# Performance work log

Hardware: AMD Instinct MI355X
Metric: run time of the kernel (lower is better)

## Reference

```python
import jax, jax.numpy as jnp
import numpy as np
from jax import lax


def _lstm_dir(x, w_ih, w_hh, b_ih, b_hh, reverse):
    """One direction of a PyTorch-style LSTM.

    x: [B, T, D]; w_ih: [4H, D]; w_hh: [4H, H]; gate order i, f, g, o.
    Returns hidden states [B, T, H] aligned with input timesteps (reverse
    scan stacks outputs back at their original positions, matching the
    backward direction of torch bidirectional LSTM).
    """
    B = x.shape[0]
    H = w_hh.shape[1]
    # Precompute input contribution for all timesteps: [T, B, 4H]
    gx = jnp.einsum('btd,gd->tbg', x, w_ih) + b_ih + b_hh

    def step(carry, g_t):
        h, c = carry
        g = g_t + h @ w_hh.T
        i, f, gg, o = jnp.split(g, 4, axis=-1)
        i = jax.nn.sigmoid(i)
        f = jax.nn.sigmoid(f)
        gg = jnp.tanh(gg)
        o = jax.nn.sigmoid(o)
        c = f * c + i * gg
        h = o * jnp.tanh(c)
        return (h, c), h

    init = (jnp.zeros((B, H), x.dtype), jnp.zeros((B, H), x.dtype))
    _, hs = lax.scan(step, init, gx, reverse=reverse)
    return jnp.swapaxes(hs, 0, 1)  # [B, T, H]


def _bilstm(x, pf, pb):
    fwd = _lstm_dir(x, *pf, reverse=False)
    bwd = _lstm_dir(x, *pb, reverse=True)
    return jnp.concatenate([fwd, bwd], axis=-1)


def setup_inputs() -> dict:
    key = jax.random.key(0)
    ks = jax.random.split(key, 32)

    def u(k, shape, H):
        bound = 1.0 / np.sqrt(H)  # torch LSTM/Linear init range
        return jax.random.uniform(k, shape, jnp.float32, -bound, bound)

    B, T, D = 512, 512, 128
    inp = {"x": jax.random.normal(ks[0], (B, T, D), jnp.float32)}
    layers = [("1", D, 32), ("2", 64, 16), ("3", 32, 8)]
    i = 1
    for name, din, H in layers:
        for d in ("f", "b"):
            inp[f"w_ih{name}_{d}"] = u(ks[i], (4 * H, din), H); i += 1
            inp[f"w_hh{name}_{d}"] = u(ks[i], (4 * H, H), H); i += 1
            inp[f"b_ih{name}_{d}"] = u(ks[i], (4 * H,), H); i += 1
            inp[f"b_hh{name}_{d}"] = u(ks[i], (4 * H,), H); i += 1
    inp["fc_w"] = u(ks[i], (6, 16), 16); i += 1
    inp["fc_b"] = u(ks[i], (6,), 16)
    return inp


def reference(x,
              w_ih1_f, w_hh1_f, b_ih1_f, b_hh1_f,
              w_ih1_b, w_hh1_b, b_ih1_b, b_hh1_b,
              w_ih2_f, w_hh2_f, b_ih2_f, b_hh2_f,
              w_ih2_b, w_hh2_b, b_ih2_b, b_hh2_b,
              w_ih3_f, w_hh3_f, b_ih3_f, b_hh3_f,
              w_ih3_b, w_hh3_b, b_ih3_b, b_hh3_b,
              fc_w, fc_b):
    h = _bilstm(x,
                (w_ih1_f, w_hh1_f, b_ih1_f, b_hh1_f),
                (w_ih1_b, w_hh1_b, b_ih1_b, b_hh1_b))  # [B,T,64]
    h = _bilstm(h,
                (w_ih2_f, w_hh2_f, b_ih2_f, b_hh2_f),
                (w_ih2_b, w_hh2_b, b_ih2_b, b_hh2_b))  # [B,T,32]
    h = _bilstm(h,
                (w_ih3_f, w_hh3_f, b_ih3_f, b_hh3_f),
                (w_ih3_b, w_hh3_b, b_ih3_b, b_hh3_b))  # [B,T,16]
    logits = h @ fc_w.T + fc_b  # [B,T,6]
    # Faithful to nn.Softmax(1): normalize over the TIME axis (dim=1).
    return jax.nn.softmax(logits, axis=1)
```

## Files before the change

### kernel.cpp

```cpp
#include <hip/hip_runtime.h>

typedef __attribute__((ext_vector_type(8))) short short8;
typedef __attribute__((ext_vector_type(4))) float f32x4;
typedef __attribute__((ext_vector_type(4))) unsigned short us4;

#define B_SZ 512
#define T_SZ 512
#define M_SZ (B_SZ * T_SZ)

#define L2E  1.4426950408889634f
#define L2E2 2.8853900817779268f

__device__ __forceinline__ unsigned short f2bf(float f) {
    union { float f; unsigned u; } v; v.f = f;
    unsigned r = v.u + 0x7FFFu + ((v.u >> 16) & 1u);
    return (unsigned short)(r >> 16);
}
__device__ __forceinline__ float bf2f(unsigned short b) {
    union { unsigned u; float f; } v; v.u = ((unsigned)b) << 16;
    return v.f;
}
__device__ __forceinline__ float rcp_(float x) { return __builtin_amdgcn_rcpf(x); }
__device__ __forceinline__ short8 cvt8(float4 a, float4 b) {
    short8 r;
    r[0] = (short)f2bf(a.x); r[1] = (short)f2bf(a.y); r[2] = (short)f2bf(a.z); r[3] = (short)f2bf(a.w);
    r[4] = (short)f2bf(b.x); r[5] = (short)f2bf(b.y); r[6] = (short)f2bf(b.z); r[7] = (short)f2bf(b.w);
    return r;
}
__device__ __forceinline__ float rdlane(float v, int lane) {
    return __int_as_float(__builtin_amdgcn_readlane(__float_as_int(v), lane));
}

__global__ __launch_bounds__(256) void prep_layer(
        const float* __restrict__ wf, const float* __restrict__ wb,
        const float* __restrict__ bif, const float* __restrict__ bhf,
        const float* __restrict__ bib, const float* __restrict__ bhb,
        unsigned short* __restrict__ wcat, float* __restrict__ bias,
        int n , int fourH, int K) {
    int H = fourH >> 2;
    int stride = gridDim.x * blockDim.x;
    for (int i = blockIdx.x * blockDim.x + threadIdx.x; i < 2 * n; i += stride) {
        int idx = (i < n) ? i : i - n;
        int gate = (idx / K) / H;
        float s = (gate == 2) ? L2E2 : L2E;
        wcat[i] = f2bf(s * ((i < n) ? wf[idx] : wb[idx]));
    }
    for (int i = blockIdx.x * blockDim.x + threadIdx.x; i < 2 * fourH; i += stride) {
        int idx = (i < fourH) ? i : i - fourH;
        int gate = idx / H;
        float s = (gate == 2) ? L2E2 : L2E;
        bias[i] = s * ((i < fourH) ? (bif[idx] + bhf[idx]) : (bib[idx] + bhb[idx]));
    }
}

__device__ __forceinline__ void store_gx(unsigned short* __restrict__ outC, int N,
                                         int b, int tl, int col, bool rev,
                                         f32x4 acc, float bv) {
    if (!rev) {
        us4 v = { f2bf(acc[0]+bv), f2bf(acc[1]+bv), f2bf(acc[2]+bv), f2bf(acc[3]+bv) };
        *(us4*)(outC + (((size_t)b * 64 + (tl >> 3)) * (size_t)N + col) * 8 + (tl & 7)) = v;
    } else {
        int p = T_SZ - 4 - tl;
        us4 v = { f2bf(acc[3]+bv), f2bf(acc[2]+bv), f2bf(acc[1]+bv), f2bf(acc[0]+bv) };
        *(us4*)(outC + (((size_t)b * 64 + (p >> 3)) * (size_t)N + col) * 8 + (p & 7)) = v;
    }
}

__global__ __launch_bounds__(256) void gemm_gx_l1(const float* __restrict__ A,
                                                  const unsigned short* __restrict__ W,
                                                  const float* __restrict__ bias,
                                                  unsigned short* __restrict__ outC) {
    constexpr int K = 128, N = 256, LDW = 136;
    __shared__ unsigned short As[64 * LDW];
    int tid = threadIdx.x;
    int slot = tid >> 6, l = tid & 63;
    int rowb = blockIdx.x * 64;

    const float* abase = A + (size_t)rowb * K;
#pragma unroll
    for (int j = 0; j < 4; j++) {
        int flat = j * 2048 + tid * 8;
        int row = flat >> 7, k = flat & 127;
        float4 a = *(const float4*)(abase + flat);
        float4 bq = *(const float4*)(abase + flat + 4);
        *(short8*)&As[row * LDW + k] = cvt8(a, bq);
    }
    __syncthreads();

    int cl = l & 15, kq = (l >> 4) * 8;
    f32x4 acc[4][4];
#pragma unroll
    for (int mt = 0; mt < 4; mt++)
#pragma unroll
        for (int nt = 0; nt < 4; nt++) acc[mt][nt] = f32x4{0, 0, 0, 0};

    const unsigned short* wp0 = W + (size_t)(slot * 64 + cl) * K + kq;
#pragma unroll
    for (int kk = 0; kk < K; kk += 32) {
        short8 af[4];
#pragma unroll
        for (int mt = 0; mt < 4; mt++)
            af[mt] = *(const short8*)&As[(mt * 16 + cl) * LDW + kq + kk];
#pragma unroll
        for (int nt = 0; nt < 4; nt++) {
            short8 bfrag = *(const short8*)(wp0 + (size_t)nt * 16 * K + kk);
#pragma unroll
            for (int mt = 0; mt < 4; mt++)
                acc[mt][nt] = __builtin_amdgcn_mfma_f32_16x16x32_bf16(af[mt], bfrag, acc[mt][nt], 0, 0, 0);
        }
    }

    int b = rowb >> 9;
    int tbase = (rowb & 511) + (l >> 4) * 4;
    bool rev = (slot >= 2);
#pragma unroll
    for (int nt = 0; nt < 4; nt++) {
        int col = slot * 64 + nt * 16 + cl;
        float bv = bias[col];
#pragma unroll
        for (int mt = 0; mt < 4; mt++)
            store_gx(outC, N, b, tbase + mt * 16, col, rev, acc[mt][nt], bv);
    }
}

template<int K, int N>
__global__ __launch_bounds__(256) void gemm_gx_split(const unsigned short* __restrict__ AF,
                                                     const unsigned short* __restrict__ AB,
                                                     const unsigned short* __restrict__ W,
                                                     const float* __restrict__ bias,
                                                     unsigned short* __restrict__ outC) {
    constexpr int TN = N / 16;
    constexpr int HALF = K / 2;
    int slot = threadIdx.x >> 6, l = threadIdx.x & 63;
    int wv = blockIdx.x * 4 + slot;
    int tg = wv / TN, tn = wv % TN;
    int rowb = tg * 64;
    int col = tn * 16 + (l & 15);
    int kq = (l >> 4) * 8;
    f32x4 acc0 = {0,0,0,0}, acc1 = {0,0,0,0}, acc2 = {0,0,0,0}, acc3 = {0,0,0,0};
    const unsigned short* wp = W + (size_t)col * K + kq;
    size_t row = (size_t)rowb + (l & 15);
    const unsigned short* baseF = AF + row * HALF;
    const unsigned short* baseB = AB + row * HALF;
#pragma unroll
    for (int kk = 0; kk < K; kk += 32) {
        int ka = kq + kk;
        const unsigned short* pb = (ka < HALF) ? (baseF + ka) : (baseB + ka - HALF);
        short8 bfrag = *(const short8*)(wp + kk);
        short8 a0 = *(const short8*)(pb);
        short8 a1 = *(const short8*)(pb + (size_t)16 * HALF);
        short8 a2 = *(const short8*)(pb + (size_t)32 * HALF);
        short8 a3 = *(const short8*)(pb + (size_t)48 * HALF);
        acc0 = __builtin_amdgcn_mfma_f32_16x16x32_bf16(a0, bfrag, acc0, 0, 0, 0);
        acc1 = __builtin_amdgcn_mfma_f32_16x16x32_bf16(a1, bfrag, acc1, 0, 0, 0);
        acc2 = __builtin_amdgcn_mfma_f32_16x16x32_bf16(a2, bfrag, acc2, 0, 0, 0);
        acc3 = __builtin_amdgcn_mfma_f32_16x16x32_bf16(a3, bfrag, acc3, 0, 0, 0);
    }
    float bv = bias[col];
    int b = rowb >> 9;
    int tbase = (rowb & 511) + (l >> 4) * 4;
    bool rev = (col >= N / 2);
    store_gx(outC, N, b, tbase,      col, rev, acc0, bv);
    store_gx(outC, N, b, tbase + 16, col, rev, acc1, bv);
    store_gx(outC, N, b, tbase + 32, col, rev, acc2, bv);
    store_gx(outC, N, b, tbase + 48, col, rev, acc3, bv);
}

template<int H>
__global__ __launch_bounds__(256, 1) void lstm_scan(const unsigned short* __restrict__ gxc,
                                                    const float* __restrict__ whhf,
                                                    const float* __restrict__ whhb,
                                                    unsigned short* __restrict__ hF,
                                                    unsigned short* __restrict__ hB) {
    constexpr int T = T_SZ;
    constexpr int G4 = 4 * H, G8 = 8 * H;
    int l = threadIdx.x & 63, slot = threadIdx.x >> 6;
    int wv = blockIdx.x * 4 + slot;
    int b = wv >> 1, dir = wv & 1;
    const float* whh = dir ? whhb : whhf;
    unsigned short* hD = dir ? hB : hF;
    __shared__ float hbuf[4][8][32];

    int jm = l & (H - 1);
    bool half = (l >= 32);
    int rA = (half ? H : 0) + jm;
    int rB = 2 * H + (half ? H : 0) + jm;

    float wA[H], wB[H];
    {
        float sB = half ? L2E : L2E2;
        const float4* wrA = (const float4*)(whh + rA * H);
        const float4* wrB = (const float4*)(whh + rB * H);
#pragma unroll
        for (int k = 0; k < H / 4; k++) {
            float4 a = wrA[k], bq = wrB[k];
            wA[4*k]=a.x*L2E; wA[4*k+1]=a.y*L2E; wA[4*k+2]=a.z*L2E; wA[4*k+3]=a.w*L2E;
            wB[4*k]=bq.x*sB; wB[4*k+1]=bq.y*sB; wB[4*k+2]=bq.z*sB; wB[4*k+3]=bq.w*sB;
        }
    }

    const unsigned short* gpA = gxc + ((size_t)b * 64 * G8 + (size_t)dir * G4 + rA) * 8;
    const unsigned short* gpB = gxc + ((size_t)b * 64 * G8 + (size_t)dir * G4 + rB) * 8;

    float c = 0.f, h = 0.f;
    short8 bufA = *(const short8*)gpA;
    short8 bufB = *(const short8*)gpB;

    for (int ch = 0; ch < T / 8; ch++) {
        short8 curA = bufA, curB = bufB;
        if (ch + 1 < T / 8) {
            bufA = *(const short8*)(gpA + (size_t)(ch + 1) * G8 * 8);
            bufB = *(const short8*)(gpB + (size_t)(ch + 1) * G8 * 8);
        }
#pragma unroll
        for (int u = 0; u < 8; u++) {
            float g0 = bf2f((unsigned short)curA[u]);
            float g1 = bf2f((unsigned short)curB[u]);

            {
                constexpr int NA = (H < 8) ? H : 8;
                float accA[NA], accB[NA];
#pragma unroll
                for (int j = 0; j < NA; j++) { accA[j] = 0.f; accB[j] = 0.f; }
#pragma unroll
                for (int k = 0; k < H; k += NA) {
#pragma unroll
                    for (int j = 0; j < NA; j++) {
                        float hk = rdlane(h, k + j);
                        accA[j] = fmaf(wA[k + j], hk, accA[j]);
                        accB[j] = fmaf(wB[k + j], hk, accB[j]);
                    }
                }
#pragma unroll
                for (int s = NA / 2; s > 0; s >>= 1)
#pragma unroll
                    for (int j = 0; j < s; j++) { accA[j] += accA[j + s]; accB[j] += accB[j + s]; }
                g0 += accA[0];
                g1 += accB[0];
            }

            float aA = rcp_(1.f + exp2f(-g0));
            float eB = exp2f(half ? -g1 : g1);
            float rB_ = rcp_(1.f + eB);
            float aB = half ? rB_ : fmaf(-2.f, rB_, 1.f);

            float xA = __shfl_xor(aA, 32, 64);
            float xB = __shfl_xor(aB, 32, 64);
            float iv = half ? xA : aA;
            float fv = half ? aA : xA;
            float gv = half ? xB : aB;
            float ov = half ? aB : xB;

            c = fmaf(fv, c, iv * gv);
            float th = fmaf(-2.f, rcp_(1.f + exp2f(c * L2E2)), 1.f);
            h = ov * th;

            if (l < H) hbuf[slot][u][l] = h;
        }
        {
            constexpr int GPT = H / 4;
            if (l < 8 * GPT) {
                int tt = l / GPT;
                int j0 = (l % GPT) * 4;
                int us = dir ? (7 - tt) : tt;
                int t  = (dir ? (T - 8 - ch * 8) : ch * 8) + tt;
                float4 hv4 = *(const float4*)&hbuf[slot][us][j0];
                us4 o = { f2bf(hv4.x), f2bf(hv4.y), f2bf(hv4.z), f2bf(hv4.w) };
                *(us4*)(hD + ((size_t)b * T + t) * H + j0) = o;
            }
        }
    }
}

__global__ __launch_bounds__(256) void fc_softmax(const unsigned short* __restrict__ h3F,
                                                  const unsigned short* __restrict__ h3B,
                                                  const float* __restrict__ fcw,
                                                  const float* __restrict__ fcb,
                                                  float* __restrict__ out) {
    constexpr int T = T_SZ;
    __shared__ float ez[T][6];
    __shared__ float ps[256][6];
    __shared__ float wf[6][16];
    __shared__ float bb[6];
    int b = blockIdx.x, tid = threadIdx.x;
    if (tid < 96) wf[tid >> 4][tid & 15] = fcw[tid];
    if (tid < 6) bb[tid] = fcb[tid];
    __syncthreads();
#pragma unroll
    for (int ii = 0; ii < 2; ii++) {
        int t = tid + ii * 256;
        short8 va = *(const short8*)(h3F + ((size_t)b * T + t) * 8);
        short8 vb = *(const short8*)(h3B + ((size_t)b * T + t) * 8);
        float hv[16];
#pragma unroll
        for (int k = 0; k < 8; k++) { hv[k] = bf2f((unsigned short)va[k]); hv[8 + k] = bf2f((unsigned short)vb[k]); }
#pragma unroll
        for (int cc = 0; cc < 6; cc++) {
            float z = bb[cc];
#pragma unroll
            for (int k = 0; k < 16; k++) z = fmaf(hv[k], wf[cc][k], z);
            ez[t][cc] = __expf(z);
        }
    }
    __syncthreads();
#pragma unroll
    for (int cc = 0; cc < 6; cc++) ps[tid][cc] = ez[tid][cc] + ez[tid + 256][cc];
    __syncthreads();
    for (int s = 128; s > 0; s >>= 1) {
        if (tid < s) {
#pragma unroll
            for (int cc = 0; cc < 6; cc++) ps[tid][cc] += ps[tid + s][cc];
        }
        __syncthreads();
    }
    float rs[6];
#pragma unroll
    for (int cc = 0; cc < 6; cc++) rs[cc] = rcp_(ps[0][cc]);
#pragma unroll
    for (int ii = 0; ii < 2; ii++) {
        int t = tid + ii * 256;
        float* op = out + ((size_t)b * T + t) * 6;
#pragma unroll
        for (int cc = 0; cc < 6; cc++) op[cc] = ez[t][cc] * rs[cc];
    }
}

extern "C" void kernel_launch(void* const* d_in, const int* in_sizes, int n_in,
                              void* d_out, int out_size, void* d_ws, size_t ws_size,
                              hipStream_t stream) {
    const float* x     = (const float*)d_in[0];
    const float* whh1f = (const float*)d_in[2];
    const float* whh1b = (const float*)d_in[6];
    const float* whh2f = (const float*)d_in[10];
    const float* whh2b = (const float*)d_in[14];
    const float* whh3f = (const float*)d_in[18];
    const float* whh3b = (const float*)d_in[22];
    const float* fcw   = (const float*)d_in[25];
    const float* fcb   = (const float*)d_in[26];

    char* ws = (char*)d_ws;
    size_t off = 0;
    auto alloc = [&](size_t bytes) -> char* {
        char* p = ws + off; off += (bytes + 255) & ~(size_t)255; return p;
    };
    unsigned short* gxc = (unsigned short*)alloc((size_t)M_SZ * 256 * 2);
    unsigned short* h1F = (unsigned short*)alloc((size_t)M_SZ * 32 * 2);
    unsigned short* h1B = (unsigned short*)alloc((size_t)M_SZ * 32 * 2);
    unsigned short* h2F = (unsigned short*)alloc((size_t)M_SZ * 16 * 2);
    unsigned short* h2B = (unsigned short*)alloc((size_t)M_SZ * 16 * 2);
    unsigned short* h3F = (unsigned short*)alloc((size_t)M_SZ * 8 * 2);
    unsigned short* h3B = (unsigned short*)alloc((size_t)M_SZ * 8 * 2);
    unsigned short* wc1 = (unsigned short*)alloc(256 * 128 * 2);
    unsigned short* wc2 = (unsigned short*)alloc(128 * 64 * 2);
    unsigned short* wc3 = (unsigned short*)alloc(64 * 32 * 2);
    float* bs1 = (float*)alloc(256 * 4);
    float* bs2 = (float*)alloc(128 * 4);
    float* bs3 = (float*)alloc(64 * 4);

    prep_layer<<<16, 256, 0, stream>>>((const float*)d_in[1], (const float*)d_in[5],
                                       (const float*)d_in[3], (const float*)d_in[4],
                                       (const float*)d_in[7], (const float*)d_in[8],
                                       wc1, bs1, 128 * 128, 128, 128);
    prep_layer<<<16, 256, 0, stream>>>((const float*)d_in[9], (const float*)d_in[13],
                                       (const float*)d_in[11], (const float*)d_in[12],
                                       (const float*)d_in[15], (const float*)d_in[16],
                                       wc2, bs2, 64 * 64, 64, 64);
    prep_layer<<<16, 256, 0, stream>>>((const float*)d_in[17], (const float*)d_in[21],
                                       (const float*)d_in[19], (const float*)d_in[20],
                                       (const float*)d_in[23], (const float*)d_in[24],
                                       wc3, bs3, 32 * 32, 32, 32);

    gemm_gx_l1<<<M_SZ / 64, 256, 0, stream>>>(x, wc1, bs1, gxc);
    lstm_scan<32><<<256, 256, 0, stream>>>(gxc, whh1f, whh1b, h1F, h1B);
    gemm_gx_split<64, 128><<<(M_SZ / 64) * 8 / 4, 256, 0, stream>>>(h1F, h1B, wc2, bs2, gxc);
    lstm_scan<16><<<256, 256, 0, stream>>>(gxc, whh2f, whh2b, h2F, h2B);
    gemm_gx_split<32, 64><<<(M_SZ / 64) * 4 / 4, 256, 0, stream>>>(h2F, h2B, wc3, bs3, gxc);
    lstm_scan<8><<<256, 256, 0, stream>>>(gxc, whh3f, whh3b, h3F, h3B);

    fc_softmax<<<B_SZ, 256, 0, stream>>>(h3F, h3B, fcw, fcb, (float*)d_out);
}
```

Measured before the change: 565.0 us.

## Use fp16 packed dot2 for LSTM recurrence with one-wave blocks and per-lane gates

The recurrent matvec in the LSTM scan now keeps weights as packed fp16 pairs and uses v_dot2 on packed hidden states broadcast via readlane, which halves the readlane and FMA count. Each lane computes all four gates for its hidden unit, removing the cross-half shuffles. Blocks shrink to a single wave, launched 1024 times, so each wave is scheduled independently. The risks are precision loss from fp16 round-toward-zero rounding of h and the weights, and redundant gate computation in lanes beyond H.

```diff
diff --git a/kernel.cpp b/kernel.cpp
--- a/kernel.cpp
+++ b/kernel.cpp
@@ -3,6 +3,9 @@
 typedef __attribute__((ext_vector_type(8))) short short8;
 typedef __attribute__((ext_vector_type(4))) float f32x4;
 typedef __attribute__((ext_vector_type(4))) unsigned short us4;
+typedef __attribute__((ext_vector_type(2))) _Float16 half2v;
+typedef __attribute__((ext_vector_type(2))) __fp16 fp16x2;
+typedef __attribute__((ext_vector_type(2))) float float2v;
 
 #define B_SZ 512
 #define T_SZ 512
@@ -27,9 +30,21 @@
     r[4] = (short)f2bf(b.x); r[5] = (short)f2bf(b.y); r[6] = (short)f2bf(b.z); r[7] = (short)f2bf(b.w);
     return r;
 }
-__device__ __forceinline__ float rdlane(float v, int lane) {
-    return __int_as_float(__builtin_amdgcn_readlane(__float_as_int(v), lane));
-}
+__device__ __forceinline__ half2v u2h(unsigned u) { union { unsigned u; half2v h; } v; v.u = u; return v.h; }
+__device__ __forceinline__ unsigned h2u(half2v h) { union { unsigned u; half2v h; } v; v.h = h; return v.u; }
+__device__ __forceinline__ half2v pkrtz(float lo, float hi) {
+    union { fp16x2 p; half2v h; } v; v.p = __builtin_amdgcn_cvt_pkrtz(lo, hi); return v.h;
+}
+
+#if __has_builtin(__builtin_amdgcn_fdot2)
+__device__ __forceinline__ float fdot2_(half2v a, half2v b, float c) {
+    return __builtin_amdgcn_fdot2(a, b, c, false);
+}
+#else
+__device__ __forceinline__ float fdot2_(half2v a, half2v b, float c) {
+    return fmaf((float)a[0], (float)b[0], fmaf((float)a[1], (float)b[1], c));
+}
+#endif
 
 __global__ __launch_bounds__(256) void prep_layer(
         const float* __restrict__ wf, const float* __restrict__ wb,
@@ -167,96 +182,104 @@
 }
 
 template<int H>
-__global__ __launch_bounds__(256, 1) void lstm_scan(const unsigned short* __restrict__ gxc,
-                                                    const float* __restrict__ whhf,
-                                                    const float* __restrict__ whhb,
-                                                    unsigned short* __restrict__ hF,
-                                                    unsigned short* __restrict__ hB) {
+__global__ __launch_bounds__(64, 1) void lstm_scan(const unsigned short* __restrict__ gxc,
+                                                   const float* __restrict__ whhf,
+                                                   const float* __restrict__ whhb,
+                                                   unsigned short* __restrict__ hF,
+                                                   unsigned short* __restrict__ hB) {
     constexpr int T = T_SZ;
-    constexpr int G4 = 4 * H, G8 = 8 * H;
-    int l = threadIdx.x & 63, slot = threadIdx.x >> 6;
-    int wv = blockIdx.x * 4 + slot;
+    constexpr int G8 = 8 * H;
+    constexpr int NP = H / 2;
+    constexpr int NC = (NP >= 8) ? 4 : ((NP >= 4) ? 2 : 1);
+    int l = threadIdx.x;
+    int wv = blockIdx.x;
     int b = wv >> 1, dir = wv & 1;
     const float* whh = dir ? whhb : whhf;
     unsigned short* hD = dir ? hB : hF;
-    __shared__ float hbuf[4][8][32];
+    __shared__ float hbuf[8][32];
 
     int jm = l & (H - 1);
-    bool half = (l >= 32);
-    int rA = (half ? H : 0) + jm;
-    int rB = 2 * H + (half ? H : 0) + jm;
-
-    float wA[H], wB[H];
+
+    half2v wI[NP], wF[NP], wG[NP], wO[NP];
     {
-        float sB = half ? L2E : L2E2;
-        const float4* wrA = (const float4*)(whh + rA * H);
-        const float4* wrB = (const float4*)(whh + rB * H);
-#pragma unroll
-        for (int k = 0; k < H / 4; k++) {
-            float4 a = wrA[k], bq = wrB[k];
-            wA[4*k]=a.x*L2E; wA[4*k+1]=a.y*L2E; wA[4*k+2]=a.z*L2E; wA[4*k+3]=a.w*L2E;
-            wB[4*k]=bq.x*sB; wB[4*k+1]=bq.y*sB; wB[4*k+2]=bq.z*sB; wB[4*k+3]=bq.w*sB;
-        }
-    }
-
-    const unsigned short* gpA = gxc + ((size_t)b * 64 * G8 + (size_t)dir * G4 + rA) * 8;
-    const unsigned short* gpB = gxc + ((size_t)b * 64 * G8 + (size_t)dir * G4 + rB) * 8;
+        const float2v* rI = (const float2v*)(whh + (0 * H + jm) * H);
+        const float2v* rF = (const float2v*)(whh + (1 * H + jm) * H);
+        const float2v* rG = (const float2v*)(whh + (2 * H + jm) * H);
+        const float2v* rO = (const float2v*)(whh + (3 * H + jm) * H);
+#pragma unroll
+        for (int k = 0; k < NP; k++) {
+            float2v vi = rI[k], vf = rF[k], vg = rG[k], vo = rO[k];
+            wI[k] = pkrtz(vi.x * L2E,  vi.y * L2E);
+            wF[k] = pkrtz(vf.x * L2E,  vf.y * L2E);
+            wG[k] = pkrtz(vg.x * L2E2, vg.y * L2E2);
+            wO[k] = pkrtz(vo.x * L2E,  vo.y * L2E);
+        }
+    }
+
+    const unsigned short* gpI = gxc + (((size_t)b * 64) * G8 + (size_t)(dir * 4 * H + 0 * H + jm)) * 8;
+    const unsigned short* gpF = gpI + (size_t)H * 8;
+    const unsigned short* gpG = gpI + (size_t)2 * H * 8;
+    const unsigned short* gpO = gpI + (size_t)3 * H * 8;
 
     float c = 0.f, h = 0.f;
-    short8 bufA = *(const short8*)gpA;
-    short8 bufB = *(const short8*)gpB;
+    unsigned pku = 0;
+    short8 bI = *(const short8*)gpI;
+    short8 bF = *(const short8*)gpF;
+    short8 bG = *(const short8*)gpG;
+    short8 bO = *(const short8*)gpO;
 
     for (int ch = 0; ch < T / 8; ch++) {
-        short8 curA = bufA, curB = bufB;
+        short8 cI = bI, cF = bF, cG = bG, cO = bO;
         if (ch + 1 < T / 8) {
-            bufA = *(const short8*)(gpA + (size_t)(ch + 1) * G8 * 8);
-            bufB = *(const short8*)(gpB + (size_t)(ch + 1) * G8 * 8);
+            size_t adv = (size_t)(ch + 1) * G8 * 8;
+            bI = *(const short8*)(gpI + adv);
+            bF = *(const short8*)(gpF + adv);
+            bG = *(const short8*)(gpG + adv);
+            bO = *(const short8*)(gpO + adv);
         }
 #pragma unroll
         for (int u = 0; u < 8; u++) {
-            float g0 = bf2f((unsigned short)curA[u]);
-            float g1 = bf2f((unsigned short)curB[u]);
-
-            {
-                constexpr int NA = (H < 8) ? H : 8;
-                float accA[NA], accB[NA];
-#pragma unroll
-                for (int j = 0; j < NA; j++) { accA[j] = 0.f; accB[j] = 0.f; }
-#pragma unroll
-                for (int k = 0; k < H; k += NA) {
-#pragma unroll
-                    for (int j = 0; j < NA; j++) {
-                        float hk = rdlane(h, k + j);
-                        accA[j] = fmaf(wA[k + j], hk, accA[j]);
-                        accB[j] = fmaf(wB[k + j], hk, accB[j]);
-                    }
+            float aI[NC], aF_[NC], aG[NC], aO[NC];
+#pragma unroll
+            for (int j = 0; j < NC; j++) { aI[j] = 0.f; aF_[j] = 0.f; aG[j] = 0.f; aO[j] = 0.f; }
+#pragma unroll
+            for (int k = 0; k < NP; k++) {
+                half2v hh = u2h((unsigned)__builtin_amdgcn_readlane((int)pku, 2 * k));
+                int cc = k & (NC - 1);
+                aI[cc]  = fdot2_(wI[k], hh, aI[cc]);
+                aF_[cc] = fdot2_(wF[k], hh, aF_[cc]);
+                aG[cc]  = fdot2_(wG[k], hh, aG[cc]);
+                aO[cc]  = fdot2_(wO[k], hh, aO[cc]);
+            }
+#pragma unroll
+            for (int s = NC / 2; s > 0; s >>= 1)
+#pragma unroll
+                for (int j = 0; j < s; j++) {
+                    aI[j] += aI[j + s]; aF_[j] += aF_[j + s];
+                    aG[j] += aG[j + s]; aO[j] += aO[j + s];
                 }
-#pragma unroll
-                for (int s = NA / 2; s > 0; s >>= 1)
-#pragma unroll
-                    for (int j = 0; j < s; j++) { accA[j] += accA[j + s]; accB[j] += accB[j + s]; }
-                g0 += accA[0];
-                g1 += accB[0];
-            }
-
-            float aA = rcp_(1.f + exp2f(-g0));
-            float eB = exp2f(half ? -g1 : g1);
-            float rB_ = rcp_(1.f + eB);
-            float aB = half ? rB_ : fmaf(-2.f, rB_, 1.f);
-
-            float xA = __shfl_xor(aA, 32, 64);
-            float xB = __shfl_xor(aB, 32, 64);
-            float iv = half ? xA : aA;
-            float fv = half ? aA : xA;
-            float gv = half ? xB : aB;
-            float ov = half ? aB : xB;
+            float gI = bf2f((unsigned short)cI[u]) + aI[0];
+            float gF = bf2f((unsigned short)cF[u]) + aF_[0];
+            float gG = bf2f((unsigned short)cG[u]) + aG[0];
+            float gO = bf2f((unsigned short)cO[u]) + aO[0];
+
+            float iv = rcp_(1.f + exp2f(-gI));
+            float fv = rcp_(1.f + exp2f(-gF));
+            float ov = rcp_(1.f + exp2f(-gO));
+            float gv = fmaf(-2.f, rcp_(1.f + exp2f(gG)), 1.f);
 
             c = fmaf(fv, c, iv * gv);
             float th = fmaf(-2.f, rcp_(1.f + exp2f(c * L2E2)), 1.f);
             h = ov * th;
 
-            if (l < H) hbuf[slot][u][l] = h;
-        }
+            float hx = __shfl_xor(h, 1, 64);
+            float plo = (l & 1) ? hx : h;
+            float phi = (l & 1) ? h : hx;
+            pku = h2u(pkrtz(plo, phi));
+
+            if (l < H) hbuf[u][l] = h;
+        }
+        __builtin_amdgcn_wave_barrier();
         {
             constexpr int GPT = H / 4;
             if (l < 8 * GPT) {
@@ -264,11 +287,12 @@
                 int j0 = (l % GPT) * 4;
                 int us = dir ? (7 - tt) : tt;
                 int t  = (dir ? (T - 8 - ch * 8) : ch * 8) + tt;
-                float4 hv4 = *(const float4*)&hbuf[slot][us][j0];
+                float4 hv4 = *(const float4*)&hbuf[us][j0];
                 us4 o = { f2bf(hv4.x), f2bf(hv4.y), f2bf(hv4.z), f2bf(hv4.w) };
                 *(us4*)(hD + ((size_t)b * T + t) * H + j0) = o;
             }
         }
+        __builtin_amdgcn_wave_barrier();
     }
 }
 
@@ -371,11 +395,11 @@
                                        wc3, bs3, 32 * 32, 32, 32);
 
     gemm_gx_l1<<<M_SZ / 64, 256, 0, stream>>>(x, wc1, bs1, gxc);
-    lstm_scan<32><<<256, 256, 0, stream>>>(gxc, whh1f, whh1b, h1F, h1B);
+    lstm_scan<32><<<1024, 64, 0, stream>>>(gxc, whh1f, whh1b, h1F, h1B);
     gemm_gx_split<64, 128><<<(M_SZ / 64) * 8 / 4, 256, 0, stream>>>(h1F, h1B, wc2, bs2, gxc);
-    lstm_scan<16><<<256, 256, 0, stream>>>(gxc, whh2f, whh2b, h2F, h2B);
+    lstm_scan<16><<<1024, 64, 0, stream>>>(gxc, whh2f, whh2b, h2F, h2B);
     gemm_gx_split<32, 64><<<(M_SZ / 64) * 4 / 4, 256, 0, stream>>>(h2F, h2B, wc3, bs3, gxc);
-    lstm_scan<8><<<256, 256, 0, stream>>>(gxc, whh3f, whh3b, h3F, h3B);
+    lstm_scan<8><<<1024, 64, 0, stream>>>(gxc, whh3f, whh3b, h3F, h3B);
 
     fc_softmax<<<B_SZ, 256, 0, stream>>>(h3F, h3B, fcw, fcb, (float*)d_out);
 }
```

Measured after the change: 934.1 us. 1.65x slower.
